# Performance work log

Measured on AMD Instinct MI355X. Metric: run time of the kernel, lower is better.

Reference implementation:

```python
import jax, jax.numpy as jnp
import numpy as np

# PEPS grid configuration (matches init_kwargs)
X, Y = 4, 4            # xnodes, ynodes
D = 6                  # bond_dim
P = 2                  # features_in (physical dim)
F = 10                 # features_out (forced by result.view([10]))
CX, CY = X // 2, Y // 2  # center node carries the output leg
BATCH = 2048


def node_labels(i, j):
    # bond labels after the physical index is contracted away; axis order: up, left, down, right, out
    labs = []
    if i > 0: labs.append(f'v{i-1}_{j}')   # up bond (shared with row i-1)
    if j > 0: labs.append(f'h{i}_{j-1}')   # left bond (shared with col j-1)
    if i < X - 1: labs.append(f'v{i}_{j}') # down bond
    if j < Y - 1: labs.append(f'h{i}_{j}') # right bond
    if (i, j) == (CX, CY): labs.append('o')  # output leg on center node
    return labs


def node_shape(i, j):
    shp = [P]  # physical axis first (input_nodes[i][j][0] ^ peps_nodes[i][j][0])
    shp += [D] * (int(i > 0) + int(j > 0) + int(i < X - 1) + int(j < Y - 1))
    if (i, j) == (CX, CY): shp.append(F)
    return tuple(shp)


def setup_inputs() -> dict:
    key = jax.random.key(0)
    keys = jax.random.split(key, X * Y + 1)
    inp = {"x": jax.random.normal(keys[0], (BATCH, X, Y, P), dtype=jnp.float32)}
    k = 1
    for i in range(X):
        for j in range(Y):
            # simple_peps uniform init with std=0.01
            inp[f"w{i}{j}"] = jax.random.uniform(keys[k], node_shape(i, j), dtype=jnp.float32, minval=-0.01, maxval=0.01)
            k += 1
    return inp


def _td(a, alabs, b, blabs):
    """Label-tracked tensordot over all shared bond labels."""
    shared = [l for l in alabs if l in blabs]
    ai = [alabs.index(l) for l in shared]
    bi = [blabs.index(l) for l in shared]
    out = jnp.tensordot(a, b, axes=(ai, bi))
    labs = [l for l in alabs if l not in shared] + [l for l in blabs if l not in shared]
    return out, labs


def _contract_sample(xs, ws):
    # xs: [X, Y, P] one sample; ws: list-of-lists of node tensors
    # 1) contract each input vector into its PEPS node over the physical axis,
    #    then L2-normalize each contracted node (as in func())
    nodes = []
    for i in range(X):
        row = []
        for j in range(Y):
            t = jnp.tensordot(xs[i, j], ws[i][j], axes=(0, 0))
            t = t / jnp.linalg.norm(t)
            row.append(t)
        nodes.append(row)
    # 2) exact contraction of the 2D network, row-by-row boundary sweep
    cur, labs = nodes[0][0], node_labels(0, 0)
    for j in range(1, Y):
        cur, labs = _td(cur, labs, nodes[0][j], node_labels(0, j))
    for i in range(1, X):
        for j in range(Y):
            cur, labs = _td(cur, labs, nodes[i][j], node_labels(i, j))
    out = cur.reshape(F)  # result.view([10])
    return out / jnp.linalg.norm(out)


def reference(x, w00, w01, w02, w03, w10, w11, w12, w13,
              w20, w21, w22, w23, w30, w31, w32, w33):
    ws = [[w00, w01, w02, w03],
          [w10, w11, w12, w13],
          [w20, w21, w22, w23],
          [w30, w31, w32, w33]]
    return jax.vmap(lambda s: _contract_sample(s, ws))(x)  # [B, F]
```

## Files before the change

kernel.cpp:

```cpp
#include <hip/hip_runtime.h>
#include <math.h>

#define NTHREADS 256

struct PW {
    const float* w[16];
    int perp[16];
};

__global__ __launch_bounds__(NTHREADS) void gram16(PW pw, float* __restrict__ g) {
    const int n = blockIdx.x;
    const float* __restrict__ W = pw.w[n];
    const int m = pw.perp[n];
    float s00 = 0.f, s01 = 0.f, s11 = 0.f;
    for (int e = threadIdx.x; e < m; e += NTHREADS) {
        float a = W[e], b = W[m + e];
        s00 += a * a; s01 += a * b; s11 += b * b;
    }
    for (int off = 32; off > 0; off >>= 1) {
        s00 += __shfl_down(s00, off, 64);
        s01 += __shfl_down(s01, off, 64);
        s11 += __shfl_down(s11, off, 64);
    }
    __shared__ float red[4][3];
    const int lane = threadIdx.x & 63, wv = threadIdx.x >> 6;
    if (lane == 0) { red[wv][0] = s00; red[wv][1] = s01; red[wv][2] = s11; }
    __syncthreads();
    if (threadIdx.x == 0) {
        float t0 = 0.f, t1 = 0.f, t2 = 0.f;
        for (int i = 0; i < 4; i++) { t0 += red[i][0]; t1 += red[i][1]; t2 += red[i][2]; }
        g[n * 3 + 0] = t0; g[n * 3 + 1] = t1; g[n * 3 + 2] = t2;
    }
}

constexpr int C1 = 0, C2 = 1296, C3 = 2592, PB = 3888;
constexpr int T00 = 4104, T01 = 4140, T10 = 4356, T11 = 4572;
constexpr int T02 = 5868, T03 = 6084, T13 = 6120, T12 = 6336;
constexpr int T30 = 7632, T20 = 7668, T31 = 7884, T21 = 8100;
constexpr int T23 = 9396, T33 = 9612, T32 = 9648;
constexpr int ARENA = 9864;

template<int M, int DST>
__device__ __forceinline__ void tmat2(float* __restrict__ lds, const float* __restrict__ W,
                                      float a0, float b0, float a1, float b1, int tid) {
    for (int e = tid; e < 2 * M; e += NTHREADS) {
        const int s = (e >= M) ? 1 : 0;
        const int idx = e - s * M;
        const float al = s ? a1 : a0;
        const float be = s ? b1 : b0;
        lds[s * ARENA + DST + idx] = al * W[idx] + be * W[M + idx];
    }
}

template<int X1, int X2, int Y1, int Y2, int U, int L, int TX,
         int AX1, int AX2, int AU, int AL,
         int BU, int BLS, int BY1, int BY2,
         int OX1, int OX2, int OY1, int OY2,
         int AOFF, int BOFF, int OOFF>
__device__ __forceinline__ void step2(float* __restrict__ lds, int tid) {
    constexpr int XB = X2 / TX;
    constexpr int TILES = X1 * XB * Y1;
    constexpr int TOT = 2 * TILES;
    for (int t = tid; t < TOT; t += NTHREADS) {
        const int sl = t / TILES;
        const int r = t - sl * TILES;
        const int x1 = r / (XB * Y1);
        const int rm = r - x1 * (XB * Y1);
        const int xb = rm / Y1;
        const int y1 = rm - xb * Y1;
        const float* __restrict__ Ab = lds + sl * ARENA + AOFF + x1 * AX1 + xb * TX * AX2;
        const float* __restrict__ Bb = lds + sl * ARENA + BOFF + y1 * BY1;
        float acc[TX][Y2];
#pragma unroll
        for (int i = 0; i < TX; i++)
#pragma unroll
            for (int t2 = 0; t2 < Y2; t2++) acc[i][t2] = 0.f;
#pragma unroll
        for (int u = 0; u < U; u++) {
#pragma unroll
            for (int l = 0; l < L; l++) {
                float a[TX];
#pragma unroll
                for (int i = 0; i < TX; i++) a[i] = Ab[i * AX2 + u * AU + l * AL];
                const float* __restrict__ Bp = Bb + u * BU + l * BLS;
#pragma unroll
                for (int t2 = 0; t2 < Y2; t2++) {
                    const float bv = Bp[t2 * BY2];
#pragma unroll
                    for (int i = 0; i < TX; i++) acc[i][t2] += a[i] * bv;
                }
            }
        }
        float* __restrict__ Ob = lds + sl * ARENA + OOFF + x1 * OX1 + xb * TX * OX2 + y1 * OY1;
#pragma unroll
        for (int i = 0; i < TX; i++)
#pragma unroll
            for (int t2 = 0; t2 < Y2; t2++) Ob[i * OX2 + t2 * OY2] = acc[i][t2];
    }
}

__global__ __launch_bounds__(NTHREADS) void peps_main(const float* __restrict__ x, PW pw,
                                                      const float* __restrict__ gram,
                                                      float* __restrict__ out) {
    __shared__ float lds[2 * ARENA];
    __shared__ float cfa[2][16], cfb[2][16];
    __shared__ float red[4][2][10];

    const int tid = threadIdx.x;
    const int s0 = blockIdx.x * 2;

    if (tid < 32) {
        const int sl = tid >> 4, n = tid & 15;
        const float a = x[(s0 + sl) * 32 + n * 2 + 0];
        const float b = x[(s0 + sl) * 32 + n * 2 + 1];
        const float g0 = gram[n * 3 + 0], g1 = gram[n * 3 + 1], g2 = gram[n * 3 + 2];
        const float inv = 1.f / sqrtf(a * a * g0 + 2.f * a * b * g1 + b * b * g2);
        cfa[sl][n] = a * inv; cfb[sl][n] = b * inv;
    }
    __syncthreads();

#define TM(M, DST, WI) tmat2<M, DST>(lds, pw.w[WI], cfa[0][WI], cfb[0][WI], cfa[1][WI], cfb[1][WI], tid)
    TM(36, T00, 0);  TM(216, T01, 1);  TM(216, T10, 4);  TM(1296, T11, 5);
    TM(216, T02, 2); TM(36, T03, 3);   TM(216, T13, 7);  TM(1296, T12, 6);
    TM(36, T30, 12); TM(216, T20, 8);  TM(216, T31, 13); TM(1296, T21, 9);
    TM(216, T23, 11); TM(36, T33, 15); TM(216, T32, 14);
#undef TM
    __syncthreads();

#define SYNC __syncthreads()
    step2<1, 6, 6, 6, 6, 1, 2,  0, 6, 1, 0,   36, 0, 6, 1,   0, 36, 6, 1,  T00, T01, PB>(lds, tid); SYNC;
    step2<1, 36, 6, 6, 6, 1, 2,  0, 1, 36, 0,  36, 0, 6, 1,   0, 36, 6, 1,  PB, T10, C1>(lds, tid); SYNC;
    step2<6, 6, 6, 6, 6, 6, 2,  36, 6, 216, 1, 216, 36, 6, 1, 216, 36, 6, 1, C1, T11, C2>(lds, tid); SYNC;
    step2<1, 36, 1, 6, 6, 1, 2,  0, 6, 1, 0,   6, 0, 0, 1,    0, 6, 0, 1,   T02, T03, PB>(lds, tid); SYNC;
    step2<1, 36, 6, 6, 6, 1, 2,  0, 6, 1, 0,   36, 0, 6, 1,   0, 36, 6, 1,  PB, T13, C1>(lds, tid); SYNC;
    step2<6, 6, 6, 6, 6, 6, 2,  36, 6, 216, 1, 36, 6, 216, 1, 216, 36, 6, 1, T12, C1, C3>(lds, tid); SYNC;
    step2<6, 6, 6, 6, 6, 6, 2,  36, 6, 216, 1, 6, 216, 36, 1, 216, 36, 6, 1, C2, C3, C1>(lds, tid); SYNC;
    step2<1, 6, 6, 6, 6, 1, 2,  0, 1, 6, 0,    6, 0, 36, 1,   0, 36, 6, 1,  T30, T20, PB>(lds, tid); SYNC;
    step2<1, 36, 6, 6, 6, 1, 2,  0, 1, 36, 0,  6, 0, 36, 1,   0, 36, 6, 1,  PB, T31, C2>(lds, tid); SYNC;
    step2<6, 6, 6, 6, 6, 6, 2,  216, 1, 36, 6, 36, 6, 216, 1, 216, 36, 6, 1, C2, T21, C3>(lds, tid); SYNC;
    step2<6, 6, 6, 6, 6, 6, 2,  6, 1, 216, 36, 216, 6, 36, 1, 216, 36, 6, 1, C1, C3, C2>(lds, tid); SYNC;
    step2<6, 6, 1, 6, 6, 1, 2,  36, 6, 1, 0,   6, 0, 0, 1,    36, 6, 0, 1,  T23, T33, PB>(lds, tid); SYNC;
    step2<6, 6, 6, 6, 6, 1, 2,  36, 6, 1, 0,   1, 0, 36, 6,   216, 1, 6, 36, PB, T32, C1>(lds, tid); SYNC;
    step2<6, 6, 6, 6, 6, 6, 2,  216, 1, 36, 6, 216, 36, 6, 1, 216, 36, 6, 1, C2, C1, C3>(lds, tid); SYNC;

    {
        const float a0 = cfa[0][10], b0 = cfb[0][10];
        const float a1 = cfa[1][10], b1 = cfb[1][10];
        const float* __restrict__ w0 = pw.w[10];
        const float* __restrict__ w1 = w0 + 12960;
        float p0[10], p1[10];
#pragma unroll
        for (int o = 0; o < 10; o++) { p0[o] = 0.f; p1[o] = 0.f; }
        for (int e = tid; e < 1296; e += NTHREADS) {
            const float E0 = lds[C3 + e];
            const float E1 = lds[ARENA + C3 + e];
            const float* __restrict__ q0 = w0 + e * 10;
            const float* __restrict__ q1 = w1 + e * 10;
#pragma unroll
            for (int o = 0; o < 10; o++) {
                const float v0 = q0[o], v1 = q1[o];
                p0[o] += E0 * (a0 * v0 + b0 * v1);
                p1[o] += E1 * (a1 * v0 + b1 * v1);
            }
        }
#pragma unroll
        for (int o = 0; o < 10; o++)
            for (int off = 32; off > 0; off >>= 1) {
                p0[o] += __shfl_down(p0[o], off, 64);
                p1[o] += __shfl_down(p1[o], off, 64);
            }
        const int lane = tid & 63, wv = tid >> 6;
        if (lane == 0) {
#pragma unroll
            for (int o = 0; o < 10; o++) { red[wv][0][o] = p0[o]; red[wv][1][o] = p1[o]; }
        }
        __syncthreads();
        if (tid < 2) {
            float r[10];
            float ss = 0.f;
#pragma unroll
            for (int o = 0; o < 10; o++) {
                r[o] = red[0][tid][o] + red[1][tid][o] + red[2][tid][o] + red[3][tid][o];
                ss += r[o] * r[o];
            }
            const float inv = 1.f / sqrtf(ss);
#pragma unroll
            for (int o = 0; o < 10; o++) out[(s0 + tid) * 10 + o] = r[o] * inv;
        }
    }
#undef SYNC
}

extern "C" void kernel_launch(void* const* d_in, const int* in_sizes, int n_in,
                              void* d_out, int out_size, void* d_ws, size_t ws_size,
                              hipStream_t stream) {
    PW pw;
    for (int k = 0; k < 16; k++) {
        pw.w[k] = (const float*)d_in[1 + k];
        pw.perp[k] = in_sizes[1 + k] / 2;
    }
    float* gram = (float*)d_ws;
    gram16<<<16, NTHREADS, 0, stream>>>(pw, gram);

    const float* x = (const float*)d_in[0];
    const int B = out_size / 10;
    peps_main<<<B / 2, NTHREADS, 0, stream>>>(x, pw, gram, (float*)d_out);
}
```

Baseline: 160.3 us.

## Restructure PEPS contraction into permuted-layout 6x6-tiled GEMMs with interleaved staging

Replaces the generic strided step2 contraction with a uniform K-major GEMM (6x6 register tiles, float2 LDS loads). Node tensors are permuted into GEMM-friendly layouts while being staged into LDS. Staging of later nodes is interleaved with earlier contraction steps, which cuts the number of barriers and shrinks the LDS arena. It also adds a 4-blocks-per-CU launch bound to raise occupancy, at the cost of register pressure from the 36-element accumulators and gather-style permuted staging.

```diff
diff --git a/kernel.cpp b/kernel.cpp
--- a/kernel.cpp
+++ b/kernel.cpp
@@ -33,75 +33,98 @@
     }
 }
 
-constexpr int C1 = 0, C2 = 1296, C3 = 2592, PB = 3888;
-constexpr int T00 = 4104, T01 = 4140, T10 = 4356, T11 = 4572;
-constexpr int T02 = 5868, T03 = 6084, T13 = 6120, T12 = 6336;
-constexpr int T30 = 7632, T20 = 7668, T31 = 7884, T21 = 8100;
-constexpr int T23 = 9396, T33 = 9612, T32 = 9648;
-constexpr int ARENA = 9864;
-
-template<int M, int DST>
-__device__ __forceinline__ void tmat2(float* __restrict__ lds, const float* __restrict__ W,
-                                      float a0, float b0, float a1, float b1, int tid) {
-    for (int e = tid; e < 2 * M; e += NTHREADS) {
-        const int s = (e >= M) ? 1 : 0;
-        const int idx = e - s * M;
-        const float al = s ? a1 : a0;
-        const float be = s ? b1 : b0;
-        lds[s * ARENA + DST + idx] = al * W[idx] + be * W[M + idx];
-    }
-}
-
-template<int X1, int X2, int Y1, int Y2, int U, int L, int TX,
-         int AX1, int AX2, int AU, int AL,
-         int BU, int BLS, int BY1, int BY2,
-         int OX1, int OX2, int OY1, int OY2,
+constexpr int SA = 0, SB = 1296, SC = 2592, SD = 3888;
+constexpr int SP = 5184, SX = 5400, SY = 5616, SZ = 5832, SU = 6048, SV = 6084;
+constexpr int ARENA = 6120;
+
+template<int TOT, int DST>
+__device__ __forceinline__ void stg_id(float* __restrict__ lds, const float* __restrict__ W,
+                                       float a0, float b0, float a1, float b1, int tid) {
+    constexpr int PAIRS = TOT / 2;
+    for (int e = tid; e < 2 * PAIRS; e += NTHREADS) {
+        const int s = (e >= PAIRS);
+        const int p = e - s * PAIRS;
+        const float al = s ? a1 : a0, be = s ? b1 : b0;
+        const float2 u0 = *reinterpret_cast<const float2*>(W + 2 * p);
+        const float2 u1 = *reinterpret_cast<const float2*>(W + TOT + 2 * p);
+        float2 rv; rv.x = al * u0.x + be * u1.x; rv.y = al * u0.y + be * u1.y;
+        *reinterpret_cast<float2*>(lds + s * ARENA + DST + 2 * p) = rv;
+    }
+}
+
+template<int D0, int D1, int D2, int D3, int S0, int S1, int S2, int S3, int DST>
+__device__ __forceinline__ void stg_pm(float* __restrict__ lds, const float* __restrict__ W,
+                                       float a0, float b0, float a1, float b1, int tid) {
+    constexpr int TOT = D0 * D1 * D2 * D3;
+    for (int e = tid; e < 2 * TOT; e += NTHREADS) {
+        const int s = (e >= TOT);
+        const int d = e - s * TOT;
+        int r = d;
+        const int i3 = r % D3; r /= D3;
+        const int i2 = r % D2; r /= D2;
+        const int i1 = r % D1;
+        const int i0 = r / D1;
+        const int src = i0 * S0 + i1 * S1 + i2 * S2 + i3 * S3;
+        const float al = s ? a1 : a0, be = s ? b1 : b0;
+        lds[s * ARENA + DST + d] = al * W[src] + be * W[TOT + src];
+    }
+}
+
+template<int M, int N, int K,
+         int NM2, int OSM1, int OSM2,
+         int NN2, int OSN1, int OSN2,
          int AOFF, int BOFF, int OOFF>
-__device__ __forceinline__ void step2(float* __restrict__ lds, int tid) {
-    constexpr int XB = X2 / TX;
-    constexpr int TILES = X1 * XB * Y1;
-    constexpr int TOT = 2 * TILES;
-    for (int t = tid; t < TOT; t += NTHREADS) {
-        const int sl = t / TILES;
-        const int r = t - sl * TILES;
-        const int x1 = r / (XB * Y1);
-        const int rm = r - x1 * (XB * Y1);
-        const int xb = rm / Y1;
-        const int y1 = rm - xb * Y1;
-        const float* __restrict__ Ab = lds + sl * ARENA + AOFF + x1 * AX1 + xb * TX * AX2;
-        const float* __restrict__ Bb = lds + sl * ARENA + BOFF + y1 * BY1;
-        float acc[TX][Y2];
-#pragma unroll
-        for (int i = 0; i < TX; i++)
-#pragma unroll
-            for (int t2 = 0; t2 < Y2; t2++) acc[i][t2] = 0.f;
-#pragma unroll
-        for (int u = 0; u < U; u++) {
-#pragma unroll
-            for (int l = 0; l < L; l++) {
-                float a[TX];
-#pragma unroll
-                for (int i = 0; i < TX; i++) a[i] = Ab[i * AX2 + u * AU + l * AL];
-                const float* __restrict__ Bp = Bb + u * BU + l * BLS;
-#pragma unroll
-                for (int t2 = 0; t2 < Y2; t2++) {
-                    const float bv = Bp[t2 * BY2];
-#pragma unroll
-                    for (int i = 0; i < TX; i++) acc[i][t2] += a[i] * bv;
-                }
-            }
-        }
-        float* __restrict__ Ob = lds + sl * ARENA + OOFF + x1 * OX1 + xb * TX * OX2 + y1 * OY1;
-#pragma unroll
-        for (int i = 0; i < TX; i++)
-#pragma unroll
-            for (int t2 = 0; t2 < Y2; t2++) Ob[i * OX2 + t2 * OY2] = acc[i][t2];
-    }
-}
-
-__global__ __launch_bounds__(NTHREADS) void peps_main(const float* __restrict__ x, PW pw,
-                                                      const float* __restrict__ gram,
-                                                      float* __restrict__ out) {
+__device__ __forceinline__ void mm(float* __restrict__ lds, int tid) {
+    constexpr int TM = 6, TN = 6;
+    constexpr int WN = N / TN;
+    constexpr int PER_S = (M / TM) * WN;
+    constexpr int TOT = 2 * PER_S;
+    for (int w = tid; w < TOT; w += NTHREADS) {
+        const int s = (w >= PER_S);
+        const int r = w - s * PER_S;
+        const int mt = r / WN;
+        const int nt = r - mt * WN;
+        const float* __restrict__ Ab = lds + s * ARENA + AOFF + mt * TM;
+        const float* __restrict__ Bb = lds + s * ARENA + BOFF + nt * TN;
+        float acc[TM][TN];
+#pragma unroll
+        for (int i = 0; i < TM; i++)
+#pragma unroll
+            for (int j = 0; j < TN; j++) acc[i][j] = 0.f;
+#pragma unroll 6
+        for (int k = 0; k < K; ++k) {
+            float a[TM], b[TN];
+            const float2* __restrict__ Ap = reinterpret_cast<const float2*>(Ab + k * M);
+            const float2* __restrict__ Bp = reinterpret_cast<const float2*>(Bb + k * N);
+#pragma unroll
+            for (int i = 0; i < TM / 2; i++) { const float2 v = Ap[i]; a[2 * i] = v.x; a[2 * i + 1] = v.y; }
+#pragma unroll
+            for (int j = 0; j < TN / 2; j++) { const float2 v = Bp[j]; b[2 * j] = v.x; b[2 * j + 1] = v.y; }
+#pragma unroll
+            for (int i = 0; i < TM; i++)
+#pragma unroll
+                for (int j = 0; j < TN; j++) acc[i][j] += a[i] * b[j];
+        }
+        float* __restrict__ Ob = lds + s * ARENA + OOFF;
+#pragma unroll
+        for (int i = 0; i < TM; i++) {
+            int m1, m2;
+            if constexpr (NM2 >= M) { m1 = 0; m2 = mt * TM + i; }
+            else                    { m1 = mt; m2 = i; }
+#pragma unroll
+            for (int j = 0; j < TN; j++) {
+                int n1, n2;
+                if constexpr (NN2 >= N) { n1 = 0; n2 = nt * TN + j; }
+                else                    { n1 = nt; n2 = j; }
+                Ob[m1 * OSM1 + m2 * OSM2 + n1 * OSN1 + n2 * OSN2] = acc[i][j];
+            }
+        }
+    }
+}
+
+__global__ __launch_bounds__(NTHREADS, 4) void peps_main(const float* __restrict__ x, PW pw,
+                                                         const float* __restrict__ gram,
+                                                         float* __restrict__ out) {
     __shared__ float lds[2 * ARENA];
     __shared__ float cfa[2][16], cfb[2][16];
     __shared__ float red[4][2][10];
@@ -119,29 +142,58 @@
     }
     __syncthreads();
 
-#define TM(M, DST, WI) tmat2<M, DST>(lds, pw.w[WI], cfa[0][WI], cfb[0][WI], cfa[1][WI], cfb[1][WI], tid)
-    TM(36, T00, 0);  TM(216, T01, 1);  TM(216, T10, 4);  TM(1296, T11, 5);
-    TM(216, T02, 2); TM(36, T03, 3);   TM(216, T13, 7);  TM(1296, T12, 6);
-    TM(36, T30, 12); TM(216, T20, 8);  TM(216, T31, 13); TM(1296, T21, 9);
-    TM(216, T23, 11); TM(36, T33, 15); TM(216, T32, 14);
-#undef TM
-    __syncthreads();
-
-#define SYNC __syncthreads()
-    step2<1, 6, 6, 6, 6, 1, 2,  0, 6, 1, 0,   36, 0, 6, 1,   0, 36, 6, 1,  T00, T01, PB>(lds, tid); SYNC;
-    step2<1, 36, 6, 6, 6, 1, 2,  0, 1, 36, 0,  36, 0, 6, 1,   0, 36, 6, 1,  PB, T10, C1>(lds, tid); SYNC;
-    step2<6, 6, 6, 6, 6, 6, 2,  36, 6, 216, 1, 216, 36, 6, 1, 216, 36, 6, 1, C1, T11, C2>(lds, tid); SYNC;
-    step2<1, 36, 1, 6, 6, 1, 2,  0, 6, 1, 0,   6, 0, 0, 1,    0, 6, 0, 1,   T02, T03, PB>(lds, tid); SYNC;
-    step2<1, 36, 6, 6, 6, 1, 2,  0, 6, 1, 0,   36, 0, 6, 1,   0, 36, 6, 1,  PB, T13, C1>(lds, tid); SYNC;
-    step2<6, 6, 6, 6, 6, 6, 2,  36, 6, 216, 1, 36, 6, 216, 1, 216, 36, 6, 1, T12, C1, C3>(lds, tid); SYNC;
-    step2<6, 6, 6, 6, 6, 6, 2,  36, 6, 216, 1, 6, 216, 36, 1, 216, 36, 6, 1, C2, C3, C1>(lds, tid); SYNC;
-    step2<1, 6, 6, 6, 6, 1, 2,  0, 1, 6, 0,    6, 0, 36, 1,   0, 36, 6, 1,  T30, T20, PB>(lds, tid); SYNC;
-    step2<1, 36, 6, 6, 6, 1, 2,  0, 1, 36, 0,  6, 0, 36, 1,   0, 36, 6, 1,  PB, T31, C2>(lds, tid); SYNC;
-    step2<6, 6, 6, 6, 6, 6, 2,  216, 1, 36, 6, 36, 6, 216, 1, 216, 36, 6, 1, C2, T21, C3>(lds, tid); SYNC;
-    step2<6, 6, 6, 6, 6, 6, 2,  6, 1, 216, 36, 216, 6, 36, 1, 216, 36, 6, 1, C1, C3, C2>(lds, tid); SYNC;
-    step2<6, 6, 1, 6, 6, 1, 2,  36, 6, 1, 0,   6, 0, 0, 1,    36, 6, 0, 1,  T23, T33, PB>(lds, tid); SYNC;
-    step2<6, 6, 6, 6, 6, 1, 2,  36, 6, 1, 0,   1, 0, 36, 6,   216, 1, 6, 36, PB, T32, C1>(lds, tid); SYNC;
-    step2<6, 6, 6, 6, 6, 6, 2,  216, 1, 36, 6, 216, 36, 6, 1, 216, 36, 6, 1, C2, C1, C3>(lds, tid); SYNC;
+#define CF(WI) cfa[0][WI], cfb[0][WI], cfa[1][WI], cfb[1][WI]
+
+    stg_pm<1, 1, 6, 6, 0, 0, 1, 6, SU>(lds, pw.w[0], CF(0), tid);
+    stg_id<216, SX>(lds, pw.w[1], CF(1), tid);
+    stg_id<216, SY>(lds, pw.w[4], CF(4), tid);
+    stg_id<1296, SA>(lds, pw.w[5], CF(5), tid);
+    __syncthreads();
+
+    mm<6, 36, 6, 6, 0, 36, 36, 0, 1, SU, SX, SP>(lds, tid);
+    stg_pm<1, 6, 6, 6, 0, 1, 36, 6, SZ>(lds, pw.w[2], CF(2), tid);
+    stg_id<36, SV>(lds, pw.w[3], CF(3), tid);
+    __syncthreads();
+
+    mm<36, 36, 6, 6, 216, 6, 6, 1, 36, SP, SY, SB>(lds, tid);
+    stg_id<216, SX>(lds, pw.w[7], CF(7), tid);
+    stg_id<36, SU>(lds, pw.w[12], CF(12), tid);
+    __syncthreads();
+
+    mm<36, 36, 36, 6, 216, 6, 6, 1, 36, SB, SA, SC>(lds, tid);
+    mm<36, 6, 6, 36, 0, 1, 6, 0, 36, SZ, SV, SP>(lds, tid);
+    stg_pm<1, 6, 6, 6, 0, 6, 36, 1, SY>(lds, pw.w[8], CF(8), tid);
+    __syncthreads();
+
+    mm<36, 36, 6, 6, 6, 216, 6, 36, 1, SP, SX, SB>(lds, tid);
+    stg_pm<6, 6, 6, 6, 216, 1, 36, 6, SA>(lds, pw.w[6], CF(6), tid);
+    __syncthreads();
+
+    mm<36, 36, 36, 6, 36, 6, 6, 216, 1, SA, SB, SD>(lds, tid);
+    stg_pm<1, 6, 6, 6, 0, 6, 36, 1, SZ>(lds, pw.w[13], CF(13), tid);
+    __syncthreads();
+
+    mm<36, 36, 36, 6, 216, 36, 6, 6, 1, SC, SD, SA>(lds, tid);
+    mm<6, 36, 6, 6, 0, 36, 36, 0, 1, SU, SY, SP>(lds, tid);
+    stg_pm<6, 6, 6, 6, 36, 6, 216, 1, SB>(lds, pw.w[9], CF(9), tid);
+    stg_pm<1, 6, 6, 6, 0, 1, 36, 6, SX>(lds, pw.w[11], CF(11), tid);
+    stg_id<36, SV>(lds, pw.w[15], CF(15), tid);
+    __syncthreads();
+
+    mm<36, 36, 6, 6, 6, 216, 6, 36, 1, SP, SZ, SC>(lds, tid);
+    stg_pm<1, 6, 6, 6, 0, 1, 36, 6, SY>(lds, pw.w[14], CF(14), tid);
+    __syncthreads();
+
+    mm<36, 36, 36, 6, 216, 6, 6, 36, 1, SC, SB, SD>(lds, tid);
+    mm<36, 6, 6, 36, 0, 1, 6, 0, 36, SX, SV, SP>(lds, tid);
+    __syncthreads();
+
+    mm<36, 36, 36, 6, 6, 216, 6, 36, 1, SA, SD, SC>(lds, tid);
+    mm<36, 36, 6, 6, 216, 1, 6, 6, 36, SP, SY, SB>(lds, tid);
+    __syncthreads();
+
+    mm<36, 36, 36, 6, 216, 36, 6, 6, 1, SC, SB, SA>(lds, tid);
+    __syncthreads();
 
     {
         const float a0 = cfa[0][10], b0 = cfb[0][10];
@@ -152,8 +204,8 @@
 #pragma unroll
         for (int o = 0; o < 10; o++) { p0[o] = 0.f; p1[o] = 0.f; }
         for (int e = tid; e < 1296; e += NTHREADS) {
-            const float E0 = lds[C3 + e];
-            const float E1 = lds[ARENA + C3 + e];
+            const float E0 = lds[SA + e];
+            const float E1 = lds[ARENA + SA + e];
             const float* __restrict__ q0 = w0 + e * 10;
             const float* __restrict__ q1 = w1 + e * 10;
 #pragma unroll
@@ -188,7 +240,7 @@
             for (int o = 0; o < 10; o++) out[(s0 + tid) * 10 + o] = r[o] * inv;
         }
     }
-#undef SYNC
+#undef CF
 }
 
 extern "C" void kernel_launch(void* const* d_in, const int* in_sizes, int n_in,
```

Measured after the change: 170.9 us. 6.6% more time.
